# Kernel optimization log

Measured on AMD Instinct MI355X. Metric: run time of the kernel, lower is better.

The kernel has to match this reference:

```python
import jax, jax.numpy as jnp
import numpy as np

N_HITS = 500_000
LATENT = 256
HITS_PER_TRACK = 10
NUM_TRACKS = N_HITS // HITS_PER_TRACK


def setup_inputs() -> dict:
    key = jax.random.key(0)
    k_h, k_w1, k_w2 = jax.random.split(key, 3)
    scale = 1.0 / np.sqrt(LATENT)
    h = jax.random.normal(k_h, (N_HITS, LATENT), dtype=jnp.float32)
    W1 = jax.random.normal(k_w1, (LATENT, LATENT), dtype=jnp.float32) * scale
    b1 = jnp.zeros((LATENT,), dtype=jnp.float32)
    w2 = jax.random.normal(k_w2, (LATENT,), dtype=jnp.float32) * scale
    b2 = jnp.zeros((), dtype=jnp.float32)
    # 10 hits per track, sorted, no empty segments
    batch_indices = (jnp.arange(N_HITS, dtype=jnp.int32) // HITS_PER_TRACK)
    return {"h": h, "W1": W1, "b1": b1, "w2": w2, "b2": b2,
            "batch_indices": batch_indices, "num_tracks": NUM_TRACKS}


def reference(h, W1, b1, w2, b2, batch_indices, num_tracks):
    # score_net: Linear -> Tanh -> Linear(->1), squeezed
    scores = jnp.tanh(h @ W1 + b1) @ w2 + b2            # (N,)
    # per-segment numerically-stable softmax
    seg_max = jax.ops.segment_max(scores, batch_indices, num_segments=num_tracks)
    e = jnp.exp(scores - seg_max[batch_indices])        # (N,)
    denom = jax.ops.segment_sum(e, batch_indices, num_segments=num_tracks)
    w = e / denom[batch_indices]                         # (N,)
    # per-segment weighted sum of h
    pooled = jax.ops.segment_sum(w[:, None] * h, batch_indices, num_segments=num_tracks)
    return pooled                                        # (num_tracks, LATENT)
```

## Files before the change

kernel.cpp:

```cpp
#include <hip/hip_runtime.h>
#include <hip/hip_bf16.h>


typedef __attribute__((ext_vector_type(8))) short short8;
typedef __attribute__((ext_vector_type(4))) float f32x4;

#define LATENT       256
#define HPT          10
#define TPB_TRACKS   40
#define ROWS_PB      (TPB_TRACKS * HPT)
#define STRIPS_PB    (ROWS_PB / 16)
#define WAVES        8
#define THREADS      (WAVES * 64)
#define W1_STRIDE    264
#define LOG2E        1.44269504088896f

__device__ __forceinline__ short bf16_rne(float x) {
    unsigned u = __float_as_uint(x);
    u += 0x7FFFu + ((u >> 16) & 1u);
    return (short)(u >> 16);
}

__device__ __forceinline__ float tanh_fast(float x) {
    float e = __builtin_amdgcn_exp2f(x * (2.0f * LOG2E));
    return 1.0f - 2.0f * __builtin_amdgcn_rcpf(e + 1.0f);
}

__global__ __launch_bounds__(THREADS, 2)
void softmax_pool_kernel(const float* __restrict__ h,
                         const float* __restrict__ W1,
                         const float* __restrict__ b1,
                         const float* __restrict__ w2,
                         float* __restrict__ out,
                         int n_hits, int num_tracks)
{
    __shared__ short w1t[256 * W1_STRIDE];
    __shared__ float sc_lds[ROWS_PB];

    const int tid  = threadIdx.x;
    const int wave = tid >> 6;
    const int lane = tid & 63;
    const int q    = lane >> 4;
    const int c    = lane & 15;
    const int blk  = blockIdx.x;

    for (int idx = tid; idx < 256 * 128; idx += THREADS) {
        int n = idx & 255;
        int k = (idx >> 8) << 1;
        float f0 = W1[(size_t)k * 256 + n];
        float f1 = W1[(size_t)(k + 1) * 256 + n];
        short2 p;
        p.x = bf16_rne(f0);
        p.y = bf16_rne(f1);
        *(short2*)&w1t[n * W1_STRIDE + k] = p;
    }
    __syncthreads();

    const int ns = (wave == 0) ? 4 : 3;

    short8 a[4][8] = {};
    #pragma unroll
    for (int st = 0; st < 4; ++st) {
        if (st < ns) {
            int strip = wave + st * 8;
            long row = (long)blk * ROWS_PB + strip * 16 + c;
            if (row >= n_hits) row = n_hits - 1;
            const float* hrow = h + (size_t)row * LATENT + q * 8;
            #pragma unroll
            for (int kt = 0; kt < 8; ++kt) {
                float4 f0 = *(const float4*)(hrow + kt * 32);
                float4 f1 = *(const float4*)(hrow + kt * 32 + 4);
                short8 v;
                v[0] = bf16_rne(f0.x); v[1] = bf16_rne(f0.y);
                v[2] = bf16_rne(f0.z); v[3] = bf16_rne(f0.w);
                v[4] = bf16_rne(f1.x); v[5] = bf16_rne(f1.y);
                v[6] = bf16_rne(f1.z); v[7] = bf16_rne(f1.w);
                a[st][kt] = v;
            }
        }
    }

    f32x4 zero4 = {0.0f, 0.0f, 0.0f, 0.0f};
    f32x4 sc[4] = {zero4, zero4, zero4, zero4};

    for (int ct = 0; ct < 16; ++ct) {
        int n = ct * 16 + c;
        const short* bbase = &w1t[n * W1_STRIDE + q * 8];
        f32x4 acc[4] = {zero4, zero4, zero4, zero4};
        #pragma unroll
        for (int kt = 0; kt < 8; ++kt) {
            short8 bf = *(const short8*)(bbase + kt * 32);
            #pragma unroll
            for (int st = 0; st < 4; ++st)
                if (st < ns)
                    acc[st] = __builtin_amdgcn_mfma_f32_16x16x32_bf16(a[st][kt], bf, acc[st], 0, 0, 0);
        }
        float b1n = b1[n];
        float w2n = w2[n];
        #pragma unroll
        for (int st = 0; st < 4; ++st) {
            if (st < ns) {
                #pragma unroll
                for (int r = 0; r < 4; ++r)
                    sc[st][r] += w2n * tanh_fast(acc[st][r] + b1n);
            }
        }
    }

    #pragma unroll
    for (int st = 0; st < 4; ++st) {
        #pragma unroll
        for (int r = 0; r < 4; ++r) {
            float v = sc[st][r];
            v += __shfl_xor(v, 1);
            v += __shfl_xor(v, 2);
            v += __shfl_xor(v, 4);
            v += __shfl_xor(v, 8);
            sc[st][r] = v;
        }
    }
    if (c == 0) {
        #pragma unroll
        for (int st = 0; st < 4; ++st) {
            if (st < ns) {
                int strip = wave + st * 8;
                float4 o;
                o.x = sc[st][0]; o.y = sc[st][1]; o.z = sc[st][2]; o.w = sc[st][3];
                *(float4*)&sc_lds[strip * 16 + q * 4] = o;
            }
        }
    }
    __syncthreads();

    if (tid < TPB_TRACKS) {
        float s[HPT];
        float m = -1e30f;
        #pragma unroll
        for (int i = 0; i < HPT; ++i) {
            s[i] = sc_lds[tid * HPT + i];
            m = fmaxf(m, s[i]);
        }
        float sum = 0.0f;
        #pragma unroll
        for (int i = 0; i < HPT; ++i) {
            s[i] = __builtin_amdgcn_exp2f((s[i] - m) * LOG2E);
            sum += s[i];
        }
        float inv = __builtin_amdgcn_rcpf(sum);
        #pragma unroll
        for (int i = 0; i < HPT; ++i)
            sc_lds[tid * HPT + i] = s[i] * inv;
    }
    __syncthreads();

    for (int t = wave; t < TPB_TRACKS; t += WAVES) {
        int tg = blk * TPB_TRACKS + t;
        if (tg >= num_tracks) continue;
        const float* hb = h + (size_t)tg * HPT * LATENT + lane * 4;
        float4 acc = {0.0f, 0.0f, 0.0f, 0.0f};
        #pragma unroll
        for (int i = 0; i < HPT; ++i) {
            float wi = sc_lds[t * HPT + i];
            float4 v = *(const float4*)(hb + (size_t)i * LATENT);
            acc.x += wi * v.x;
            acc.y += wi * v.y;
            acc.z += wi * v.z;
            acc.w += wi * v.w;
        }
        *(float4*)(out + (size_t)tg * LATENT + lane * 4) = acc;
    }
}

extern "C" void kernel_launch(void* const* d_in, const int* in_sizes, int n_in,
                              void* d_out, int out_size, void* d_ws, size_t ws_size,
                              hipStream_t stream) {
    const float* h  = (const float*)d_in[0];
    const float* W1 = (const float*)d_in[1];
    const float* b1 = (const float*)d_in[2];
    const float* w2 = (const float*)d_in[3];
    float* out = (float*)d_out;

    int n_hits     = in_sizes[0] / LATENT;
    int num_tracks = out_size / LATENT;
    int blocks     = (num_tracks + TPB_TRACKS - 1) / TPB_TRACKS;

    softmax_pool_kernel<<<blocks, THREADS, 0, stream>>>(h, W1, b1, w2, out, n_hits, num_tracks);
}
```

Before: 841.1 us.

## Pre-convert W1 to bf16 once and stream it in chunks to shrink LDS

A separate pre-kernel writes W1 as a transposed, padded bf16 image into the workspace. The main kernel then streams that image into a 64-column LDS chunk with async global-to-LDS copies, instead of every block converting the full 256x256 matrix. Blocks shrink to 16 tracks and 5 waves, each wave handling 2 row strips, which cuts LDS per block and raises the occupancy target to 4 blocks. The cost is four extra barrier-separated chunk loads per block, more blocks each re-reading W1 from L2, and an added kernel launch.

```diff
diff --git a/kernel.cpp b/kernel.cpp
--- a/kernel.cpp
+++ b/kernel.cpp
@@ -5,15 +5,19 @@
 typedef __attribute__((ext_vector_type(8))) short short8;
 typedef __attribute__((ext_vector_type(4))) float f32x4;
 
-#define LATENT       256
-#define HPT          10
-#define TPB_TRACKS   40
-#define ROWS_PB      (TPB_TRACKS * HPT)
-#define STRIPS_PB    (ROWS_PB / 16)
-#define WAVES        8
-#define THREADS      (WAVES * 64)
-#define W1_STRIDE    264
-#define LOG2E        1.44269504088896f
+#define LATENT      256
+#define HPT         10
+#define TPB_TRACKS  16
+#define ROWS_PB     (TPB_TRACKS * HPT)
+#define STRIPS_PB   (ROWS_PB / 16)
+#define WAVES       5
+#define THREADS     (WAVES * 64)
+#define NCHUNK      4
+#define CHUNK_N     64
+#define W1_STRIDE   264
+#define CHUNK_BYTES (CHUNK_N * W1_STRIDE * 2)
+#define IMG_BYTES   (256 * W1_STRIDE * 2)
+#define LOG2E       1.44269504088896f
 
 __device__ __forceinline__ short bf16_rne(float x) {
     unsigned u = __float_as_uint(x);
@@ -26,15 +30,36 @@
     return 1.0f - 2.0f * __builtin_amdgcn_rcpf(e + 1.0f);
 }
 
-__global__ __launch_bounds__(THREADS, 2)
+__device__ __forceinline__ void async_copy16(const void* g, void* l) {
+    __builtin_amdgcn_global_load_lds(
+        (const __attribute__((address_space(1))) unsigned int*)g,
+        (__attribute__((address_space(3))) unsigned int*)l, 16, 0, 0);
+}
+
+__global__ __launch_bounds__(256)
+void convert_w1_kernel(const float* __restrict__ W1, short* __restrict__ img) {
+    int idx = blockIdx.x * 256 + threadIdx.x;
+    int p = idx >> 8;
+    int n = idx & 255;
+    short2 v; v.x = 0; v.y = 0;
+    if (p < 128) {
+        int k = p * 2;
+        v.x = bf16_rne(W1[(size_t)k * 256 + n]);
+        v.y = bf16_rne(W1[(size_t)(k + 1) * 256 + n]);
+    }
+    *(short2*)&img[(size_t)n * W1_STRIDE + p * 2] = v;
+}
+
+__global__ __launch_bounds__(THREADS, 4)
 void softmax_pool_kernel(const float* __restrict__ h,
                          const float* __restrict__ W1,
                          const float* __restrict__ b1,
                          const float* __restrict__ w2,
+                         const short* __restrict__ img,
                          float* __restrict__ out,
-                         int n_hits, int num_tracks)
+                         int n_hits, int num_tracks, int use_ws)
 {
-    __shared__ short w1t[256 * W1_STRIDE];
+    __shared__ __align__(16) short w1t[CHUNK_N * W1_STRIDE];
     __shared__ float sc_lds[ROWS_PB];
 
     const int tid  = threadIdx.x;
@@ -44,91 +69,87 @@
     const int c    = lane & 15;
     const int blk  = blockIdx.x;
 
-    for (int idx = tid; idx < 256 * 128; idx += THREADS) {
-        int n = idx & 255;
-        int k = (idx >> 8) << 1;
-        float f0 = W1[(size_t)k * 256 + n];
-        float f1 = W1[(size_t)(k + 1) * 256 + n];
-        short2 p;
-        p.x = bf16_rne(f0);
-        p.y = bf16_rne(f1);
-        *(short2*)&w1t[n * W1_STRIDE + k] = p;
-    }
-    __syncthreads();
-
-    const int ns = (wave == 0) ? 4 : 3;
-
-    short8 a[4][8] = {};
+    short8 a[2][8];
     #pragma unroll
-    for (int st = 0; st < 4; ++st) {
-        if (st < ns) {
-            int strip = wave + st * 8;
-            long row = (long)blk * ROWS_PB + strip * 16 + c;
-            if (row >= n_hits) row = n_hits - 1;
-            const float* hrow = h + (size_t)row * LATENT + q * 8;
+    for (int st = 0; st < 2; ++st) {
+        const int strip = wave + st * WAVES;
+        size_t row = (size_t)blk * ROWS_PB + (size_t)strip * 16 + c;
+        if (row >= (size_t)n_hits) row = n_hits - 1;
+        const float* hrow = h + row * LATENT + q * 8;
+        #pragma unroll
+        for (int kt = 0; kt < 8; ++kt) {
+            float4 f0 = *(const float4*)(hrow + kt * 32);
+            float4 f1 = *(const float4*)(hrow + kt * 32 + 4);
+            short8 v;
+            v[0] = bf16_rne(f0.x); v[1] = bf16_rne(f0.y);
+            v[2] = bf16_rne(f0.z); v[3] = bf16_rne(f0.w);
+            v[4] = bf16_rne(f1.x); v[5] = bf16_rne(f1.y);
+            v[6] = bf16_rne(f1.z); v[7] = bf16_rne(f1.w);
+            a[st][kt] = v;
+        }
+    }
+
+    f32x4 zero4 = {0.0f, 0.0f, 0.0f, 0.0f};
+    f32x4 sc0 = zero4, sc1 = zero4;
+
+    for (int chunk = 0; chunk < NCHUNK; ++chunk) {
+        __syncthreads();
+        if (use_ws) {
+            const char* src = (const char*)img + (size_t)chunk * CHUNK_BYTES;
+            char* dst = (char*)w1t;
+            for (int off = wave * 1024; off < CHUNK_BYTES; off += WAVES * 1024)
+                async_copy16(src + off + lane * 16, dst + off);
+        } else {
+            for (int idx = tid; idx < CHUNK_N * 132; idx += THREADS) {
+                int nl = idx & (CHUNK_N - 1);
+                int p  = idx >> 6;
+                short2 v; v.x = 0; v.y = 0;
+                if (p < 128) {
+                    int k = p * 2;
+                    int n = chunk * CHUNK_N + nl;
+                    v.x = bf16_rne(W1[(size_t)k * 256 + n]);
+                    v.y = bf16_rne(W1[(size_t)(k + 1) * 256 + n]);
+                }
+                *(short2*)&w1t[nl * W1_STRIDE + p * 2] = v;
+            }
+        }
+        __syncthreads();
+
+        #pragma unroll
+        for (int ct = 0; ct < 4; ++ct) {
+            const int n = chunk * CHUNK_N + ct * 16 + c;
+            const short* bbase = &w1t[(ct * 16 + c) * W1_STRIDE + q * 8];
+            f32x4 acc0 = zero4, acc1 = zero4;
             #pragma unroll
             for (int kt = 0; kt < 8; ++kt) {
-                float4 f0 = *(const float4*)(hrow + kt * 32);
-                float4 f1 = *(const float4*)(hrow + kt * 32 + 4);
-                short8 v;
-                v[0] = bf16_rne(f0.x); v[1] = bf16_rne(f0.y);
-                v[2] = bf16_rne(f0.z); v[3] = bf16_rne(f0.w);
-                v[4] = bf16_rne(f1.x); v[5] = bf16_rne(f1.y);
-                v[6] = bf16_rne(f1.z); v[7] = bf16_rne(f1.w);
-                a[st][kt] = v;
+                short8 bf = *(const short8*)(bbase + kt * 32);
+                acc0 = __builtin_amdgcn_mfma_f32_16x16x32_bf16(a[0][kt], bf, acc0, 0, 0, 0);
+                acc1 = __builtin_amdgcn_mfma_f32_16x16x32_bf16(a[1][kt], bf, acc1, 0, 0, 0);
             }
-        }
-    }
-
-    f32x4 zero4 = {0.0f, 0.0f, 0.0f, 0.0f};
-    f32x4 sc[4] = {zero4, zero4, zero4, zero4};
-
-    for (int ct = 0; ct < 16; ++ct) {
-        int n = ct * 16 + c;
-        const short* bbase = &w1t[n * W1_STRIDE + q * 8];
-        f32x4 acc[4] = {zero4, zero4, zero4, zero4};
-        #pragma unroll
-        for (int kt = 0; kt < 8; ++kt) {
-            short8 bf = *(const short8*)(bbase + kt * 32);
+            float b1n = b1[n];
+            float w2n = w2[n];
             #pragma unroll
-            for (int st = 0; st < 4; ++st)
-                if (st < ns)
-                    acc[st] = __builtin_amdgcn_mfma_f32_16x16x32_bf16(a[st][kt], bf, acc[st], 0, 0, 0);
-        }
-        float b1n = b1[n];
-        float w2n = w2[n];
-        #pragma unroll
-        for (int st = 0; st < 4; ++st) {
-            if (st < ns) {
-                #pragma unroll
-                for (int r = 0; r < 4; ++r)
-                    sc[st][r] += w2n * tanh_fast(acc[st][r] + b1n);
+            for (int r = 0; r < 4; ++r) {
+                sc0[r] += w2n * tanh_fast(acc0[r] + b1n);
+                sc1[r] += w2n * tanh_fast(acc1[r] + b1n);
             }
         }
     }
 
     #pragma unroll
-    for (int st = 0; st < 4; ++st) {
-        #pragma unroll
-        for (int r = 0; r < 4; ++r) {
-            float v = sc[st][r];
-            v += __shfl_xor(v, 1);
-            v += __shfl_xor(v, 2);
-            v += __shfl_xor(v, 4);
-            v += __shfl_xor(v, 8);
-            sc[st][r] = v;
-        }
+    for (int r = 0; r < 4; ++r) {
+        float v0 = sc0[r], v1 = sc1[r];
+        v0 += __shfl_xor(v0, 1); v0 += __shfl_xor(v0, 2);
+        v0 += __shfl_xor(v0, 4); v0 += __shfl_xor(v0, 8);
+        v1 += __shfl_xor(v1, 1); v1 += __shfl_xor(v1, 2);
+        v1 += __shfl_xor(v1, 4); v1 += __shfl_xor(v1, 8);
+        sc0[r] = v0; sc1[r] = v1;
     }
     if (c == 0) {
-        #pragma unroll
-        for (int st = 0; st < 4; ++st) {
-            if (st < ns) {
-                int strip = wave + st * 8;
-                float4 o;
-                o.x = sc[st][0]; o.y = sc[st][1]; o.z = sc[st][2]; o.w = sc[st][3];
-                *(float4*)&sc_lds[strip * 16 + q * 4] = o;
-            }
-        }
+        float4 o0; o0.x = sc0[0]; o0.y = sc0[1]; o0.z = sc0[2]; o0.w = sc0[3];
+        *(float4*)&sc_lds[wave * 16 + q * 4] = o0;
+        float4 o1; o1.x = sc1[0]; o1.y = sc1[1]; o1.z = sc1[2]; o1.w = sc1[3];
+        *(float4*)&sc_lds[(wave + WAVES) * 16 + q * 4] = o1;
     }
     __syncthreads();
 
@@ -184,5 +205,12 @@
     int num_tracks = out_size / LATENT;
     int blocks     = (num_tracks + TPB_TRACKS - 1) / TPB_TRACKS;
 
-    softmax_pool_kernel<<<blocks, THREADS, 0, stream>>>(h, W1, b1, w2, out, n_hits, num_tracks);
-}
+    int use_ws = (ws_size >= (size_t)IMG_BYTES) ? 1 : 0;
+    short* img = (short*)d_ws;
+
+    if (use_ws)
+        convert_w1_kernel<<<132, 256, 0, stream>>>(W1, img);
+
+    softmax_pool_kernel<<<blocks, THREADS, 0, stream>>>(h, W1, b1, w2, img, out,
+                                                        n_hits, num_tracks, use_ws);
+}
```

New measurement: 847.0 us. No clear change (+0.7%).
